# Performance work log

Hardware: AMD Instinct MI355X
Metric: run time of the kernel (lower is better)

The kernel has to match this reference:

```python
import jax, jax.numpy as jnp
import numpy as np
from jax.scipy.special import logsumexp

B, T, M = 64, 1024, 128  # batch, seq_len, tag_set_size


def setup_inputs() -> dict:
    key = jax.random.key(0)
    kP, kA, kY, kL = jax.random.split(key, 4)
    P = jax.random.normal(kP, (B, T, M), dtype=jnp.float32)
    A = jax.random.normal(kA, (M + 1, M), dtype=jnp.float32)  # rows 0..M-1: transitions, row M: start
    Y = jax.random.randint(kY, (B, T, 1), 0, M).astype(jnp.int32)
    L = jax.random.randint(kL, (B,), 1, T + 1).astype(jnp.int32)  # lengths in [1, T]
    return {"P": P, "A": A, "Y": Y, "L": L}


def _crf_losses(P, A, Y, L):
    b, t, m = P.shape
    y = Y[:, :, 0]                      # [B,T] int labels
    A_trans, A_start = A[:-1], A[-1]    # [M,M], [M]
    b_idx = jnp.arange(b)

    # step 0
    S0 = P[:, 0] + A_start              # [B,M] forward scores
    sY0 = P[b_idx, 0, y[:, 0]] + A_start[y[:, 0]]  # gold path score at t=0
    loss0 = logsumexp(S0, axis=1) - sY0

    Pt = jnp.swapaxes(P, 0, 1)          # [T,B,M] time-major for scan
    yt = jnp.swapaxes(y, 0, 1)          # [T,B]

    def step(carry, xs):
        S_prev, sY_prev = carry
        P_k, y_prev, y_k = xs           # [B,M], [B], [B]
        # S_k[b,j] = logsumexp_i( S_prev[b,i] + A_trans[i,j] + P_k[b,j] )
        S_k = logsumexp(S_prev[:, :, None] + A_trans[None, :, :] + P_k[:, None, :], axis=1)
        sY = sY_prev + P_k[b_idx, y_k] + A_trans[y_prev, y_k]
        loss = logsumexp(S_k, axis=1) - sY
        return (S_k, sY), loss

    (_, _), losses = jax.lax.scan(step, (S0, sY0), (Pt[1:], yt[:-1], yt[1:]))
    all_losses = jnp.concatenate([loss0[None], losses], axis=0)  # [T,B]
    # pick loss at the true sequence end (L-1) for each batch element
    return all_losses[L - 1, b_idx]


def reference(P, A, Y, L):
    return _crf_losses(P, A, Y, L)
```

## Files before the change

kernel.cpp:

```cpp
#include <hip/hip_runtime.h>

#define T_LEN 1024
#define M_DIM 128
#define B_NUM 64

__global__ __launch_bounds__(256, 1) void crf_fwd(
    const float* __restrict__ P, const float* __restrict__ A,
    const int* __restrict__ Y, const int* __restrict__ L,
    float* __restrict__ out)
{
  const int b    = blockIdx.x;
  const int tid  = threadIdx.x;
  const int lane = tid & 63;
  const int wid  = tid >> 6;
  const int igrp = lane & 7;
  const int jql  = (lane >> 3) & 7;
  const int jq   = wid * 8 + jql;
  const int j0   = jq * 4;

  __shared__ __align__(16) float u_lds[2][M_DIM];
  __shared__ __align__(16) float red[4];
  __shared__ float red_sum[4];
  __shared__ float sY_sh[4];

  const int Lb = L[b];
  const float* Pb = P + (size_t)b * T_LEN * M_DIM;
  const int*   Yb = Y + b * T_LEN;

#define BARRIER_RELAXED() do { \
    asm volatile("s_waitcnt lgkmcnt(0)" ::: "memory"); \
    __builtin_amdgcn_s_barrier(); } while (0)

  float w[64];
  #pragma unroll
  for (int k = 0; k < 4; ++k) {
    const int slot = (k + igrp) & 3;
    #pragma unroll
    for (int e = 0; e < 4; ++e) {
      const int i = igrp * 16 + slot * 4 + e;
      #pragma unroll
      for (int jj = 0; jj < 4; ++jj)
        w[(k * 4 + e) * 4 + jj] = __expf(A[i * M_DIM + j0 + jj]);
    }
  }

  float mySY = 0.f;
  for (int tt = tid; tt < Lb; tt += 256) {
    int yt = Yb[tt];
    float term = Pb[tt * M_DIM + yt];
    term += (tt == 0) ? A[M_DIM * M_DIM + yt] : A[Yb[tt - 1] * M_DIM + yt];
    mySY += term;
  }
  #pragma unroll
  for (int d = 1; d < 64; d <<= 1) mySY += __shfl_xor(mySY, d);
  if (lane == 0) sY_sh[wid] = mySY;

  float4 p0 = *(const float4*)(Pb + j0);
  float4 as = *(const float4*)(A + M_DIM * M_DIM + j0);
  float4 un;
  un.x = __expf(p0.x + as.x); un.y = __expf(p0.y + as.y);
  un.z = __expf(p0.z + as.z); un.w = __expf(p0.w + as.w);
  if (igrp == 0) *(float4*)&u_lds[0][j0] = un;
  {
    float zm = fmaxf(fmaxf(un.x, un.y), fmaxf(un.z, un.w));
    #pragma unroll
    for (int d = 8; d < 64; d <<= 1) zm = fmaxf(zm, __shfl_xor(zm, d));
    if (lane == 0) red[wid] = zm;
  }
  float C = 0.f;
  float4 p_cur = *(const float4*)(Pb + M_DIM + j0);
  if (Lb == 1) {
    float zs = (igrp == 0) ? (un.x + un.y) + (un.z + un.w) : 0.f;
    #pragma unroll
    for (int d = 1; d < 64; d <<= 1) zs += __shfl_xor(zs, d);
    if (lane == 0) red_sum[wid] = zs;
  }
  __syncthreads();

  if (Lb == 1) {
    if (tid == 0) {
      float s  = (red_sum[0] + red_sum[1]) + (red_sum[2] + red_sum[3]);
      float sy = (sY_sh[0] + sY_sh[1]) + (sY_sh[2] + sY_sh[3]);
      out[b] = __logf(s) - sy;
    }
    return;
  }

#define CRF_STEP(S, MODE, PNEXT)                                           \
  {                                                                        \
    float4 ep;                                                             \
    ep.x = __expf(p_cur.x); ep.y = __expf(p_cur.y);                        \
    ep.z = __expf(p_cur.z); ep.w = __expf(p_cur.w);                        \
    if ((MODE) == 1) {                                                     \
      float4 rz = *(const float4*)red;                                     \
      float Z = fmaxf(fmaxf(rz.x, rz.y), fmaxf(rz.z, rz.w));               \
      C += __logf(Z);                                                      \
      float iZ = __builtin_amdgcn_rcpf(Z);                                 \
      ep.x *= iZ; ep.y *= iZ; ep.z *= iZ; ep.w *= iZ;                      \
    }                                                                      \
    const float4* u4 = (const float4*)(u_lds[cur]);                        \
    float acc[4] = {0.f, 0.f, 0.f, 0.f};                                   \
    _Pragma("unroll")                                                      \
    for (int k = 0; k < 4; ++k) {                                          \
      float4 uu = u4[igrp * 4 + ((k + igrp) & 3)];                         \
      const float ue[4] = {uu.x, uu.y, uu.z, uu.w};                        \
      _Pragma("unroll")                                                    \
      for (int e = 0; e < 4; ++e) {                                        \
        _Pragma("unroll")                                                  \
        for (int jj = 0; jj < 4; ++jj)                                     \
          acc[jj] = fmaf(ue[e], w[(k * 4 + e) * 4 + jj], acc[jj]);         \
      }                                                                    \
    }                                                                      \
    _Pragma("unroll")                                                      \
    for (int jj = 0; jj < 4; ++jj) {                                       \
      acc[jj] += __shfl_xor(acc[jj], 1);                                   \
      acc[jj] += __shfl_xor(acc[jj], 2);                                   \
      acc[jj] += __shfl_xor(acc[jj], 4);                                   \
    }                                                                      \
    un.x = acc[0] * ep.x; un.y = acc[1] * ep.y;                            \
    un.z = acc[2] * ep.z; un.w = acc[3] * ep.w;                            \
    if (igrp == 0) *(float4*)&u_lds[cur ^ 1][j0] = un;                     \
    const bool last_ = (tb + (S) == Lb - 1);                               \
    if (last_) {                                                           \
      float zs = (igrp == 0) ? (un.x + un.y) + (un.z + un.w) : 0.f;        \
      _Pragma("unroll")                                                    \
      for (int d = 1; d < 64; d <<= 1) zs += __shfl_xor(zs, d);            \
      if (lane == 0) red_sum[wid] = zs;                                    \
    } else if ((MODE) == 2) {                                              \
      float zm = fmaxf(fmaxf(un.x, un.y), fmaxf(un.z, un.w));              \
      _Pragma("unroll")                                                    \
      for (int d = 8; d < 64; d <<= 1) zm = fmaxf(zm, __shfl_xor(zm, d));  \
      if (lane == 0) red[wid] = zm;                                        \
    }                                                                      \
    BARRIER_RELAXED();                                                     \
    if (last_) goto finish;                                                \
    p_cur = (PNEXT);                                                       \
    cur ^= 1;                                                              \
  }

  {
    int cur = 0;
    int tb  = 1;
    const float* Pq = Pb + j0;
    for (;;) {
      float4 pn0, pn1, pn2, pn3, pn4, pn5, pn6, pn7;
      {
        int r;
        r = tb + 1; r = r < T_LEN ? r : T_LEN - 1; pn0 = *(const float4*)(Pq + r * M_DIM);
        r = tb + 2; r = r < T_LEN ? r : T_LEN - 1; pn1 = *(const float4*)(Pq + r * M_DIM);
        r = tb + 3; r = r < T_LEN ? r : T_LEN - 1; pn2 = *(const float4*)(Pq + r * M_DIM);
        r = tb + 4; r = r < T_LEN ? r : T_LEN - 1; pn3 = *(const float4*)(Pq + r * M_DIM);
        r = tb + 5; r = r < T_LEN ? r : T_LEN - 1; pn4 = *(const float4*)(Pq + r * M_DIM);
        r = tb + 6; r = r < T_LEN ? r : T_LEN - 1; pn5 = *(const float4*)(Pq + r * M_DIM);
        r = tb + 7; r = r < T_LEN ? r : T_LEN - 1; pn6 = *(const float4*)(Pq + r * M_DIM);
        r = tb + 8; r = r < T_LEN ? r : T_LEN - 1; pn7 = *(const float4*)(Pq + r * M_DIM);
      }
      CRF_STEP(0, 1, pn0)
      CRF_STEP(1, 0, pn1)
      CRF_STEP(2, 0, pn2)
      CRF_STEP(3, 2, pn3)
      CRF_STEP(4, 1, pn4)
      CRF_STEP(5, 0, pn5)
      CRF_STEP(6, 0, pn6)
      CRF_STEP(7, 2, pn7)
      tb += 8;
    }
  }

finish:
  if (tid == 0) {
    float s  = (red_sum[0] + red_sum[1]) + (red_sum[2] + red_sum[3]);
    float sy = (sY_sh[0] + sY_sh[1]) + (sY_sh[2] + sY_sh[3]);
    out[b] = __logf(s) + C - sy;
  }
}

extern "C" void kernel_launch(void* const* d_in, const int* in_sizes, int n_in,
                              void* d_out, int out_size, void* d_ws, size_t ws_size,
                              hipStream_t stream) {
  const float* P = (const float*)d_in[0];
  const float* A = (const float*)d_in[1];
  const int*   Y = (const int*)d_in[2];
  const int*   L = (const int*)d_in[3];
  float* o = (float*)d_out;
  hipLaunchKernelGGL(crf_fwd, dim3(B_NUM), dim3(256), 0, stream, P, A, Y, L, o);
}
```

Baseline: 432.5 us.

## Split CRF recurrence over 512 threads and reduce partial sums with DPP

The block grows from 256 to 512 threads, so each thread covers 8 source states instead of 16. That halves the per-thread FMA chain and weight registers in each time step. The 16-lane partial-sum reduction now uses DPP quad_perm and mirror adds instead of shuffle-based xor exchanges, which shortens the cross-lane reduction latency on the serial critical path. In exchange, every per-step barrier now has to synchronise 8 waves, and the max and sum reductions are spread over more LDS slots.

New measurement: 410.7 us. 5.0% less time.

```diff
diff --git a/kernel.cpp b/kernel.cpp
--- a/kernel.cpp
+++ b/kernel.cpp
@@ -4,7 +4,13 @@
 #define M_DIM 128
 #define B_NUM 64
 
-__global__ __launch_bounds__(256, 1) void crf_fwd(
+template<int CTRL>
+__device__ __forceinline__ float dpp_add(float x) {
+  int y = __builtin_amdgcn_update_dpp(0, __float_as_int(x), CTRL, 0xf, 0xf, true);
+  return x + __int_as_float(y);
+}
+
+__global__ __launch_bounds__(512, 2) void crf_fwd(
     const float* __restrict__ P, const float* __restrict__ A,
     const int* __restrict__ Y, const int* __restrict__ L,
     float* __restrict__ out)
@@ -13,15 +19,18 @@
   const int tid  = threadIdx.x;
   const int lane = tid & 63;
   const int wid  = tid >> 6;
-  const int igrp = lane & 7;
-  const int jql  = (lane >> 3) & 7;
-  const int jq   = wid * 8 + jql;
+  const int igrp = lane & 15;
+  const int jql  = (lane >> 4) & 3;
+  const int jq   = wid * 4 + jql;
   const int j0   = jq * 4;
+  const int s    = (igrp >> 2) & 1;
+  const int f0   = igrp * 2 + s;
+  const int f1   = igrp * 2 + (s ^ 1);
 
   __shared__ __align__(16) float u_lds[2][M_DIM];
-  __shared__ __align__(16) float red[4];
-  __shared__ float red_sum[4];
-  __shared__ float sY_sh[4];
+  __shared__ __align__(16) float red[8];
+  __shared__ float red_sum[8];
+  __shared__ float sY_sh[8];
 
   const int Lb = L[b];
   const float* Pb = P + (size_t)b * T_LEN * M_DIM;
@@ -31,21 +40,20 @@
     asm volatile("s_waitcnt lgkmcnt(0)" ::: "memory"); \
     __builtin_amdgcn_s_barrier(); } while (0)
 
-  float w[64];
+  float w[32];
   #pragma unroll
-  for (int k = 0; k < 4; ++k) {
-    const int slot = (k + igrp) & 3;
+  for (int q = 0; q < 2; ++q) {
     #pragma unroll
     for (int e = 0; e < 4; ++e) {
-      const int i = igrp * 16 + slot * 4 + e;
+      const int i = igrp * 8 + ((s ^ q) << 2) + e;
       #pragma unroll
       for (int jj = 0; jj < 4; ++jj)
-        w[(k * 4 + e) * 4 + jj] = __expf(A[i * M_DIM + j0 + jj]);
+        w[q * 16 + e * 4 + jj] = __expf(A[i * M_DIM + j0 + jj]);
     }
   }
 
   float mySY = 0.f;
-  for (int tt = tid; tt < Lb; tt += 256) {
+  for (int tt = tid; tt < Lb; tt += 512) {
     int yt = Yb[tt];
     float term = Pb[tt * M_DIM + yt];
     term += (tt == 0) ? A[M_DIM * M_DIM + yt] : A[Yb[tt - 1] * M_DIM + yt];
@@ -63,8 +71,8 @@
   if (igrp == 0) *(float4*)&u_lds[0][j0] = un;
   {
     float zm = fmaxf(fmaxf(un.x, un.y), fmaxf(un.z, un.w));
-    #pragma unroll
-    for (int d = 8; d < 64; d <<= 1) zm = fmaxf(zm, __shfl_xor(zm, d));
+    zm = fmaxf(zm, __shfl_xor(zm, 16));
+    zm = fmaxf(zm, __shfl_xor(zm, 32));
     if (lane == 0) red[wid] = zm;
   }
   float C = 0.f;
@@ -79,9 +87,10 @@
 
   if (Lb == 1) {
     if (tid == 0) {
-      float s  = (red_sum[0] + red_sum[1]) + (red_sum[2] + red_sum[3]);
-      float sy = (sY_sh[0] + sY_sh[1]) + (sY_sh[2] + sY_sh[3]);
-      out[b] = __logf(s) - sy;
+      float s_ = 0.f, sy = 0.f;
+      #pragma unroll
+      for (int q = 0; q < 8; ++q) { s_ += red_sum[q]; sy += sY_sh[q]; }
+      out[b] = __logf(s_) - sy;
     }
     return;
   }
@@ -92,30 +101,42 @@
     ep.x = __expf(p_cur.x); ep.y = __expf(p_cur.y);                        \
     ep.z = __expf(p_cur.z); ep.w = __expf(p_cur.w);                        \
     if ((MODE) == 1) {                                                     \
-      float4 rz = *(const float4*)red;                                     \
-      float Z = fmaxf(fmaxf(rz.x, rz.y), fmaxf(rz.z, rz.w));               \
+      float4 ra = *(const float4*)&red[0];                                 \
+      float4 rb = *(const float4*)&red[4];                                 \
+      float Z = fmaxf(fmaxf(fmaxf(ra.x, ra.y), fmaxf(ra.z, ra.w)),         \
+                      fmaxf(fmaxf(rb.x, rb.y), fmaxf(rb.z, rb.w)));        \
       C += __logf(Z);                                                      \
       float iZ = __builtin_amdgcn_rcpf(Z);                                 \
       ep.x *= iZ; ep.y *= iZ; ep.z *= iZ; ep.w *= iZ;                      \
     }                                                                      \
     const float4* u4 = (const float4*)(u_lds[cur]);                        \
     float acc[4] = {0.f, 0.f, 0.f, 0.f};                                   \
-    _Pragma("unroll")                                                      \
-    for (int k = 0; k < 4; ++k) {                                          \
-      float4 uu = u4[igrp * 4 + ((k + igrp) & 3)];                         \
+    {                                                                      \
+      float4 uu = u4[f0];                                                  \
       const float ue[4] = {uu.x, uu.y, uu.z, uu.w};                        \
       _Pragma("unroll")                                                    \
-      for (int e = 0; e < 4; ++e) {                                        \
+      for (int e = 0; e < 4; ++e)                                          \
         _Pragma("unroll")                                                  \
         for (int jj = 0; jj < 4; ++jj)                                     \
-          acc[jj] = fmaf(ue[e], w[(k * 4 + e) * 4 + jj], acc[jj]);         \
-      }                                                                    \
+          acc[jj] = fmaf(ue[e], w[e * 4 + jj], acc[jj]);                   \
+    }                                                                      \
+    {                                                                      \
+      float4 uu = u4[f1];                                                  \
+      const float ue[4] = {uu.x, uu.y, uu.z, uu.w};                        \
+      _Pragma("unroll")                                                    \
+      for (int e = 0; e < 4; ++e)                                          \
+        _Pragma("unroll")                                                  \
+        for (int jj = 0; jj < 4; ++jj)                                     \
+          acc[jj] = fmaf(ue[e], w[16 + e * 4 + jj], acc[jj]);              \
     }                                                                      \
     _Pragma("unroll")                                                      \
     for (int jj = 0; jj < 4; ++jj) {                                       \
-      acc[jj] += __shfl_xor(acc[jj], 1);                                   \
-      acc[jj] += __shfl_xor(acc[jj], 2);                                   \
-      acc[jj] += __shfl_xor(acc[jj], 4);                                   \
+      float a = acc[jj];                                                   \
+      a = dpp_add<0xB1>(a);                                                \
+      a = dpp_add<0x4E>(a);                                                \
+      a = dpp_add<0x141>(a);                                               \
+      a = dpp_add<0x140>(a);                                               \
+      acc[jj] = a;                                                         \
     }                                                                      \
     un.x = acc[0] * ep.x; un.y = acc[1] * ep.y;                            \
     un.z = acc[2] * ep.z; un.w = acc[3] * ep.w;                            \
@@ -128,8 +149,8 @@
       if (lane == 0) red_sum[wid] = zs;                                    \
     } else if ((MODE) == 2) {                                              \
       float zm = fmaxf(fmaxf(un.x, un.y), fmaxf(un.z, un.w));              \
-      _Pragma("unroll")                                                    \
-      for (int d = 8; d < 64; d <<= 1) zm = fmaxf(zm, __shfl_xor(zm, d));  \
+      zm = fmaxf(zm, __shfl_xor(zm, 16));                                  \
+      zm = fmaxf(zm, __shfl_xor(zm, 32));                                  \
       if (lane == 0) red[wid] = zm;                                        \
     }                                                                      \
     BARRIER_RELAXED();                                                     \
@@ -169,9 +190,10 @@
 
 finish:
   if (tid == 0) {
-    float s  = (red_sum[0] + red_sum[1]) + (red_sum[2] + red_sum[3]);
-    float sy = (sY_sh[0] + sY_sh[1]) + (sY_sh[2] + sY_sh[3]);
-    out[b] = __logf(s) + C - sy;
+    float s_ = 0.f, sy = 0.f;
+    #pragma unroll
+    for (int q = 0; q < 8; ++q) { s_ += red_sum[q]; sy += sY_sh[q]; }
+    out[b] = __logf(s_) + C - sy;
   }
 }
 
@@ -183,5 +205,5 @@
   const int*   Y = (const int*)d_in[2];
   const int*   L = (const int*)d_in[3];
   float* o = (float*)d_out;
-  hipLaunchKernelGGL(crf_fwd, dim3(B_NUM), dim3(256), 0, stream, P, A, Y, L, o);
+  hipLaunchKernelGGL(crf_fwd, dim3(B_NUM), dim3(512), 0, stream, P, A, Y, L, o);
 }
```

## Use fp16 packed dot products for CRF forward with per-step DPP max renormalisation

Applied to the files above, without the earlier changes.

Stores exp(A) weights and the forward vector u as packed fp16 and computes the matvec with fdot2, giving each thread one output column with the i-range split across two half-waves. Renormalisation now uses the previous step's max every step, taken from a double-buffered reduction array and computed with DPP row operations instead of shuffles. A fixed 1/256 scale keeps values in fp16 range. This cuts the FMA count and the cross-lane reduction work on the serial critical path, at the cost of fp16 precision in the recurrence.

Result: slower. 474.7 us (+9.8%).

```diff
diff --git a/kernel.cpp b/kernel.cpp
--- a/kernel.cpp
+++ b/kernel.cpp
@@ -3,6 +3,22 @@
 #define T_LEN 1024
 #define M_DIM 128
 #define B_NUM 64
+
+typedef _Float16 h2 __attribute__((ext_vector_type(2)));
+
+#if __has_builtin(__builtin_amdgcn_fdot2)
+#define DOT2(a, b, c) __builtin_amdgcn_fdot2((a), (b), (c), false)
+#else
+__device__ __forceinline__ float DOT2(h2 a, h2 b, float c) {
+  return fmaf((float)a.x, (float)b.x, fmaf((float)a.y, (float)b.y, c));
+}
+#endif
+
+template<int CTRL>
+__device__ __forceinline__ float dppmov(float x) {
+  int y = __builtin_amdgcn_update_dpp(0, __float_as_int(x), CTRL, 0xf, 0xf, true);
+  return __int_as_float(y);
+}
 
 __global__ __launch_bounds__(256, 1) void crf_fwd(
     const float* __restrict__ P, const float* __restrict__ A,
@@ -13,15 +29,15 @@
   const int tid  = threadIdx.x;
   const int lane = tid & 63;
   const int wid  = tid >> 6;
-  const int igrp = lane & 7;
-  const int jql  = (lane >> 3) & 7;
-  const int jq   = wid * 8 + jql;
-  const int j0   = jq * 4;
-
-  __shared__ __align__(16) float u_lds[2][M_DIM];
-  __shared__ __align__(16) float red[4];
-  __shared__ float red_sum[4];
-  __shared__ float sY_sh[4];
+  const int jl   = lane & 31;
+  const int half = lane >> 5;
+  const int j    = wid * 32 + jl;
+
+  __shared__ __align__(16) h2    u_lds[2][80];
+  __shared__ __align__(16) float red[2][4];
+  __shared__ __align__(16) float red_sum[4];
+  __shared__ __align__(16) float sY_sh[4];
+  __shared__ __align__(16) float boot[4];
 
   const int Lb = L[b];
   const float* Pb = P + (size_t)b * T_LEN * M_DIM;
@@ -31,18 +47,22 @@
     asm volatile("s_waitcnt lgkmcnt(0)" ::: "memory"); \
     __builtin_amdgcn_s_barrier(); } while (0)
 
-  float w[64];
+  h2 wpk[32];
   #pragma unroll
-  for (int k = 0; k < 4; ++k) {
-    const int slot = (k + igrp) & 3;
+  for (int k = 0; k < 8; ++k) {
     #pragma unroll
     for (int e = 0; e < 4; ++e) {
-      const int i = igrp * 16 + slot * 4 + e;
-      #pragma unroll
-      for (int jj = 0; jj < 4; ++jj)
-        w[(k * 4 + e) * 4 + jj] = __expf(A[i * M_DIM + j0 + jj]);
+      const int i = (half * 32 + k * 4 + e) * 2;
+      h2 hv;
+      hv.x = (_Float16)__expf(A[i * M_DIM + j]);
+      hv.y = (_Float16)__expf(A[(i + 1) * M_DIM + j]);
+      wpk[k * 4 + e] = hv;
     }
   }
+
+  const int wslot_m = wid * 16 + (jl >> 1);
+  const int wslot   = wslot_m < 32 ? wslot_m : 36 + (wslot_m - 32);
+  const bool writer = (half == 0) && !(jl & 1);
 
   float mySY = 0.f;
   for (int tt = tid; tt < Lb; tt += 256) {
@@ -55,82 +75,75 @@
   for (int d = 1; d < 64; d <<= 1) mySY += __shfl_xor(mySY, d);
   if (lane == 0) sY_sh[wid] = mySY;
 
-  float4 p0 = *(const float4*)(Pb + j0);
-  float4 as = *(const float4*)(A + M_DIM * M_DIM + j0);
-  float4 un;
-  un.x = __expf(p0.x + as.x); un.y = __expf(p0.y + as.y);
-  un.z = __expf(p0.z + as.z); un.w = __expf(p0.w + as.w);
-  if (igrp == 0) *(float4*)&u_lds[0][j0] = un;
+  float s0 = Pb[j] + A[M_DIM * M_DIM + j];
   {
-    float zm = fmaxf(fmaxf(un.x, un.y), fmaxf(un.z, un.w));
+    float mm = s0;
     #pragma unroll
-    for (int d = 8; d < 64; d <<= 1) zm = fmaxf(zm, __shfl_xor(zm, d));
-    if (lane == 0) red[wid] = zm;
-  }
-  float C = 0.f;
-  float4 p_cur = *(const float4*)(Pb + M_DIM + j0);
+    for (int d = 1; d <= 16; d <<= 1) mm = fmaxf(mm, __shfl_xor(mm, d));
+    if (lane == 0) boot[wid] = mm;
+  }
+  if (tid < 4) red[1][tid] = 1.0f;
+  __syncthreads();
+  float C = fmaxf(fmaxf(boot[0], boot[1]), fmaxf(boot[2], boot[3]));
+  float un = __expf(s0 - C);
+  {
+    float nb = __shfl_xor(un, 1);
+    if (writer) {
+      h2 hv; hv.x = (_Float16)un; hv.y = (_Float16)nb;
+      u_lds[0][wslot] = hv;
+    }
+  }
+  float p_cur = Pb[M_DIM + j];
   if (Lb == 1) {
-    float zs = (igrp == 0) ? (un.x + un.y) + (un.z + un.w) : 0.f;
+    float zs = un;
     #pragma unroll
-    for (int d = 1; d < 64; d <<= 1) zs += __shfl_xor(zs, d);
+    for (int d = 1; d <= 16; d <<= 1) zs += __shfl_xor(zs, d);
     if (lane == 0) red_sum[wid] = zs;
   }
   __syncthreads();
-
-  if (Lb == 1) {
-    if (tid == 0) {
-      float s  = (red_sum[0] + red_sum[1]) + (red_sum[2] + red_sum[3]);
-      float sy = (sY_sh[0] + sY_sh[1]) + (sY_sh[2] + sY_sh[3]);
-      out[b] = __logf(s) - sy;
-    }
-    return;
-  }
-
-#define CRF_STEP(S, MODE, PNEXT)                                           \
+  if (Lb == 1) goto finish;
+
+#define CRF_STEP(S, PAR, PNEXT)                                            \
   {                                                                        \
-    float4 ep;                                                             \
-    ep.x = __expf(p_cur.x); ep.y = __expf(p_cur.y);                        \
-    ep.z = __expf(p_cur.z); ep.w = __expf(p_cur.w);                        \
-    if ((MODE) == 1) {                                                     \
-      float4 rz = *(const float4*)red;                                     \
-      float Z = fmaxf(fmaxf(rz.x, rz.y), fmaxf(rz.z, rz.w));               \
-      C += __logf(Z);                                                      \
-      float iZ = __builtin_amdgcn_rcpf(Z);                                 \
-      ep.x *= iZ; ep.y *= iZ; ep.z *= iZ; ep.w *= iZ;                      \
-    }                                                                      \
     const float4* u4 = (const float4*)(u_lds[cur]);                        \
-    float acc[4] = {0.f, 0.f, 0.f, 0.f};                                   \
+    float4 rz = *(const float4*)(&red[PAR][0]);                            \
+    float Z  = fmaxf(fmaxf(rz.x, rz.y), fmaxf(rz.z, rz.w));                \
+    float ep = __expf(p_cur) * __builtin_amdgcn_rcpf(Z) * 0.00390625f;     \
+    C += __logf(Z) + 5.54517744f;                      \
+    float acc0 = 0.f, acc1 = 0.f, acc2 = 0.f, acc3 = 0.f;                  \
     _Pragma("unroll")                                                      \
-    for (int k = 0; k < 4; ++k) {                                          \
-      float4 uu = u4[igrp * 4 + ((k + igrp) & 3)];                         \
-      const float ue[4] = {uu.x, uu.y, uu.z, uu.w};                        \
-      _Pragma("unroll")                                                    \
-      for (int e = 0; e < 4; ++e) {                                        \
-        _Pragma("unroll")                                                  \
-        for (int jj = 0; jj < 4; ++jj)                                     \
-          acc[jj] = fmaf(ue[e], w[(k * 4 + e) * 4 + jj], acc[jj]);         \
+    for (int k = 0; k < 8; ++k) {                                          \
+      float4 uu = u4[half * 9 + k];                                        \
+      acc0 = DOT2(__builtin_bit_cast(h2, uu.x), wpk[k * 4 + 0], acc0);     \
+      acc1 = DOT2(__builtin_bit_cast(h2, uu.y), wpk[k * 4 + 1], acc1);     \
+      acc2 = DOT2(__builtin_bit_cast(h2, uu.z), wpk[k * 4 + 2], acc2);     \
+      acc3 = DOT2(__builtin_bit_cast(h2, uu.w), wpk[k * 4 + 3], acc3);     \
+    }                                                                      \
+    float v = (acc0 + acc1) + (acc2 + acc3);                               \
+    v += __shfl_xor(v, 32);                                                \
+    un = v * ep;                                                           \
+    {                                                                      \
+      float nb = __shfl_xor(un, 1);                                        \
+      if (writer) {                                                        \
+        h2 hv; hv.x = (_Float16)un; hv.y = (_Float16)nb;                   \
+        u_lds[cur ^ 1][wslot] = hv;                                        \
       }                                                                    \
     }                                                                      \
-    _Pragma("unroll")                                                      \
-    for (int jj = 0; jj < 4; ++jj) {                                       \
-      acc[jj] += __shfl_xor(acc[jj], 1);                                   \
-      acc[jj] += __shfl_xor(acc[jj], 2);                                   \
-      acc[jj] += __shfl_xor(acc[jj], 4);                                   \
-    }                                                                      \
-    un.x = acc[0] * ep.x; un.y = acc[1] * ep.y;                            \
-    un.z = acc[2] * ep.z; un.w = acc[3] * ep.w;                            \
-    if (igrp == 0) *(float4*)&u_lds[cur ^ 1][j0] = un;                     \
+    {                     \
+      float zm = un;                                                       \
+      zm = fmaxf(zm, dppmov<0xB1>(zm));                          \
+      zm = fmaxf(zm, dppmov<0x4E>(zm));                          \
+      zm = fmaxf(zm, dppmov<0x141>(zm));          \
+      zm = fmaxf(zm, dppmov<0x140>(zm));               \
+      zm = fmaxf(zm, dppmov<0x142>(zm));     \
+      if (lane == 16) red[(PAR) ^ 1][wid] = zm;                            \
+    }                                                                      \
     const bool last_ = (tb + (S) == Lb - 1);                               \
     if (last_) {                                                           \
-      float zs = (igrp == 0) ? (un.x + un.y) + (un.z + un.w) : 0.f;        \
+      float zs = un;                                                       \
       _Pragma("unroll")                                                    \
-      for (int d = 1; d < 64; d <<= 1) zs += __shfl_xor(zs, d);            \
+      for (int d = 1; d <= 16; d <<= 1) zs += __shfl_xor(zs, d);           \
       if (lane == 0) red_sum[wid] = zs;                                    \
-    } else if ((MODE) == 2) {                                              \
-      float zm = fmaxf(fmaxf(un.x, un.y), fmaxf(un.z, un.w));              \
-      _Pragma("unroll")                                                    \
-      for (int d = 8; d < 64; d <<= 1) zm = fmaxf(zm, __shfl_xor(zm, d));  \
-      if (lane == 0) red[wid] = zm;                                        \
     }                                                                      \
     BARRIER_RELAXED();                                                     \
     if (last_) goto finish;                                                \
@@ -141,28 +154,28 @@
   {
     int cur = 0;
     int tb  = 1;
-    const float* Pq = Pb + j0;
     for (;;) {
-      float4 pn0, pn1, pn2, pn3, pn4, pn5, pn6, pn7;
+      float pn0, pn1, pn2, pn3, pn4, pn5, pn6, pn7;
       {
+        const float* Pq = Pb + j;
         int r;
-        r = tb + 1; r = r < T_LEN ? r : T_LEN - 1; pn0 = *(const float4*)(Pq + r * M_DIM);
-        r = tb + 2; r = r < T_LEN ? r : T_LEN - 1; pn1 = *(const float4*)(Pq + r * M_DIM);
-        r = tb + 3; r = r < T_LEN ? r : T_LEN - 1; pn2 = *(const float4*)(Pq + r * M_DIM);
-        r = tb + 4; r = r < T_LEN ? r : T_LEN - 1; pn3 = *(const float4*)(Pq + r * M_DIM);
-        r = tb + 5; r = r < T_LEN ? r : T_LEN - 1; pn4 = *(const float4*)(Pq + r * M_DIM);
-        r = tb + 6; r = r < T_LEN ? r : T_LEN - 1; pn5 = *(const float4*)(Pq + r * M_DIM);
-        r = tb + 7; r = r < T_LEN ? r : T_LEN - 1; pn6 = *(const float4*)(Pq + r * M_DIM);
-        r = tb + 8; r = r < T_LEN ? r : T_LEN - 1; pn7 = *(const float4*)(Pq + r * M_DIM);
+        r = tb + 1; r = r < T_LEN ? r : T_LEN - 1; pn0 = Pq[r * M_DIM];
+        r = tb + 2; r = r < T_LEN ? r : T_LEN - 1; pn1 = Pq[r * M_DIM];
+        r = tb + 3; r = r < T_LEN ? r : T_LEN - 1; pn2 = Pq[r * M_DIM];
+        r = tb + 4; r = r < T_LEN ? r : T_LEN - 1; pn3 = Pq[r * M_DIM];
+        r = tb + 5; r = r < T_LEN ? r : T_LEN - 1; pn4 = Pq[r * M_DIM];
+        r = tb + 6; r = r < T_LEN ? r : T_LEN - 1; pn5 = Pq[r * M_DIM];
+        r = tb + 7; r = r < T_LEN ? r : T_LEN - 1; pn6 = Pq[r * M_DIM];
+        r = tb + 8; r = r < T_LEN ? r : T_LEN - 1; pn7 = Pq[r * M_DIM];
       }
       CRF_STEP(0, 1, pn0)
       CRF_STEP(1, 0, pn1)
-      CRF_STEP(2, 0, pn2)
-      CRF_STEP(3, 2, pn3)
+      CRF_STEP(2, 1, pn2)
+      CRF_STEP(3, 0, pn3)
       CRF_STEP(4, 1, pn4)
       CRF_STEP(5, 0, pn5)
-      CRF_STEP(6, 0, pn6)
-      CRF_STEP(7, 2, pn7)
+      CRF_STEP(6, 1, pn6)
+      CRF_STEP(7, 0, pn7)
       tb += 8;
     }
   }
```
